# Optimization experiments

Measured on AMD Instinct MI355X. Metric: run time of the kernel, lower is better.

The kernel has to match this reference:

```python
import jax, jax.numpy as jnp
import numpy as np

B, C_IN, C_OUT, H, MAXN = 128, 32, 32, 4096, 6


def setup_inputs() -> dict:
    key = jax.random.key(0)
    ks = jax.random.split(key, 6)
    x = jax.random.normal(ks[0], (B, C_IN, H), dtype=jnp.float32)
    weight = jax.random.normal(ks[1], (C_OUT, C_IN, MAXN + 1), dtype=jnp.float32) * 0.05
    bias = jax.random.normal(ks[2], (C_OUT,), dtype=jnp.float32) * 0.05
    gamma = jnp.ones((C_OUT,), dtype=jnp.float32)
    beta = jnp.zeros((C_OUT,), dtype=jnp.float32)
    # hex neighbor table; -1 marks invalid (boundary) neighbors
    neighbors = jax.random.randint(ks[3], (H, MAXN), -1, H, dtype=jnp.int64)
    return {"x": x, "weight": weight, "bias": bias, "gamma": gamma,
            "beta": beta, "neighbors": neighbors, "groups": 1}


def reference(x, weight, bias, gamma, beta, neighbors, groups):
    Bsz, Cin, Hn = x.shape
    Cout, _, K = weight.shape  # K = total_inputs = max_neighbors + 1
    G = groups
    # global std normalization (torch std: unbiased, ddof=1)
    x = x / (jnp.std(x, ddof=1) + 1e-5)
    valid = (neighbors >= 0)                      # [H, K-1]
    idx = jnp.clip(neighbors, 0, None)
    nbr = x[:, :, idx] * valid.astype(x.dtype)[None, None]   # [B,C,H,K-1]
    allv = jnp.concatenate([x[..., None], nbr], axis=3)      # [B,C,H,K]
    allv = allv.reshape(Bsz, G, Cin // G, Hn, K)
    w = weight.reshape(G, Cout // G, Cin // G, K)
    out = jnp.einsum('bgihk,goik->bgoh', allv, w).reshape(Bsz, Cout, Hn)
    total_valid = valid.sum(axis=1).astype(out.dtype)[None, None] + 1.0  # [1,1,H]
    out = out / (total_valid + 1e-6)
    out = out + bias[None, :, None]
    # BatchNorm1d in training mode: per-channel over (batch, hex), biased var
    mean = out.mean(axis=(0, 2), keepdims=True)
    var = out.var(axis=(0, 2), keepdims=True)
    out = gamma[None, :, None] * (out - mean) * jax.lax.rsqrt(var + 1e-5) + beta[None, :, None]
    return out
```

## Files before the change

kernel.cpp:

```cpp
#include <hip/hip_runtime.h>
#include <stdint.h>
#include <stddef.h>

#define BSZ 128
#define CIN 32
#define COUT 32
#define HN 4096
#define K7 7
#define NTOT (BSZ*CIN*HN)
#define NBH  (BSZ*HN)

typedef __attribute__((ext_vector_type(8))) short short8;
typedef __attribute__((ext_vector_type(4))) float f32x4;

#define WS_XT   0
#define WS_WT   33554432
#define WS_NBR  33568768
#define WS_INVD 33699840
#define WS_DSP  33716224
#define WS_OST  33720320
#define WS_OSTP 33720576

__device__ __forceinline__ unsigned short f32_to_bf16(float f){
    union { float f; uint32_t u; } v; v.f = f;
    uint32_t u = v.u;
    return (unsigned short)((u + 0x7FFFu + ((u >> 16) & 1u)) >> 16);
}

__global__ void kprep(const int* __restrict__ nbr,
                      int* __restrict__ nbr_pack,
                      float* __restrict__ invd,
                      double* __restrict__ dsp,
                      float* __restrict__ ostatp){
    int t = blockIdx.x*blockDim.x + threadIdx.x;
    if (t < 512) dsp[t] = 0.0;
    #pragma unroll
    for (int j = 0; j < 4; j++) ostatp[t*4 + j] = 0.0f;
    if (t < HN){
        int cnt = 0;
        int pk[8];
        pk[0] = t;
        #pragma unroll
        for (int j = 0; j < 6; j++){
            int iv = nbr[t*6 + j];
            if (iv >= HN) iv = HN - 1;
            if (iv >= 0) cnt++; else iv = -1;
            pk[1+j] = iv;
        }
        pk[7] = 0;
        #pragma unroll
        for (int j = 0; j < 8; j++) nbr_pack[t*8 + j] = pk[j];
        invd[t] = 1.0f / ((float)cnt + 1.0f + 1e-6f);
    }
}

__global__ void ktrans(const float* __restrict__ x,
                       unsigned short* __restrict__ xt,
                       double* __restrict__ dsp){
    __shared__ float tile[32][65];
    __shared__ double red[8];
    int b  = blockIdx.x >> 6;
    int h0 = (blockIdx.x & 63) << 6;
    int t  = threadIdx.x;
    int hh = t & 63;
    int cq = t >> 6;
    double ds = 0.0, ds2 = 0.0;
    #pragma unroll
    for (int rep = 0; rep < 8; rep++){
        int c = rep*4 + cq;
        float v = x[((size_t)(b*32 + c))*HN + h0 + hh];
        tile[c][hh] = v;
        double dv = (double)v;
        ds += dv; ds2 += dv*dv;
    }
    #pragma unroll
    for (int off = 32; off; off >>= 1){
        ds  += __shfl_down(ds,  off);
        ds2 += __shfl_down(ds2, off);
    }
    int lane = t & 63, wv = t >> 6;
    if (lane == 0){ red[wv] = ds; red[4+wv] = ds2; }
    __syncthreads();
    if (t == 0){
        int slot = blockIdx.x & 255;
        atomicAdd(&dsp[slot*2],     red[0]+red[1]+red[2]+red[3]);
        atomicAdd(&dsp[slot*2 + 1], red[4]+red[5]+red[6]+red[7]);
    }
    int hw = t >> 2;
    int cg = (t & 3) * 8;
    alignas(16) unsigned short tmp[8];
    #pragma unroll
    for (int j = 0; j < 8; j++) tmp[j] = f32_to_bf16(tile[cg + j][hw]);
    *(uint4*)(xt + ((size_t)(b*HN + h0 + hw))*32 + cg) = *(const uint4*)tmp;
}

__global__ void kwt(const float* __restrict__ w,
                    const double* __restrict__ dsp,
                    unsigned short* __restrict__ wt){
    __shared__ double sred[8];
    __shared__ float sinv;
    int t = threadIdx.x;
    double d0 = dsp[t*2], d1 = dsp[t*2 + 1];
    #pragma unroll
    for (int off = 32; off; off >>= 1){
        d0 += __shfl_down(d0, off);
        d1 += __shfl_down(d1, off);
    }
    int lane = t & 63, wv = t >> 6;
    if (lane == 0){ sred[wv] = d0; sred[4+wv] = d1; }
    __syncthreads();
    if (t == 0){
        double sum   = sred[0]+sred[1]+sred[2]+sred[3];
        double sumsq = sred[4]+sred[5]+sred[6]+sred[7];
        double mean = sum / (double)NTOT;
        double var  = (sumsq - (double)NTOT*mean*mean) / (double)(NTOT - 1);
        sinv = 1.0f / ((float)sqrt(var) + 1e-5f);
    }
    __syncthreads();
    float inv_s = sinv;
    for (int i = t; i < COUT*K7*CIN; i += blockDim.x){
        int o  = i / (K7*CIN);
        int kk = (i / CIN) % K7;
        int c  = i % CIN;
        float val = w[(o*CIN + c)*K7 + kk] * inv_s;
        wt[i] = f32_to_bf16(val);
    }
}

__global__ __launch_bounds__(256) void kconv(
    const unsigned short* __restrict__ xt,
    const unsigned short* __restrict__ wt,
    const int* __restrict__ nbrp,
    const float* __restrict__ invd,
    const float* __restrict__ bias,
    float* __restrict__ out,
    float* __restrict__ ostatp)
{
    int lane = threadIdx.x & 63;
    int wv   = threadIdx.x >> 6;
    int wgid = blockIdx.x*4 + wv;
    int n    = lane & 15;
    int quad = lane >> 4;

    short8 af[2][K7];
    #pragma unroll
    for (int mt = 0; mt < 2; mt++){
        int o = n + 16*mt;
        #pragma unroll
        for (int kk = 0; kk < K7; kk++)
            af[mt][kk] = *(const short8*)(wt + (size_t)(o*K7 + kk)*CIN + quad*8);
    }
    float bias8[2][4];
    #pragma unroll
    for (int mt = 0; mt < 2; mt++)
        #pragma unroll
        for (int r = 0; r < 4; r++)
            bias8[mt][r] = bias[mt*16 + quad*4 + r];

    float sacc[8]  = {0,0,0,0,0,0,0,0};
    float sacc2[8] = {0,0,0,0,0,0,0,0};
    const short8 zero8 = {0,0,0,0,0,0,0,0};

    for (int tilei = wgid; tilei < (NBH/16); tilei += 8192){
        int b  = tilei >> 8;
        int h0 = (tilei & 255) << 4;
        int h  = h0 + n;
        float idv = invd[h];
        const int* np = nbrp + h*8;

        short8 bfr[K7];
        #pragma unroll
        for (int kk = 0; kk < K7; kk++){
            int row  = np[kk];
            int rowc = row < 0 ? 0 : row;
            bfr[kk] = *(const short8*)(xt + ((size_t)(b*HN + rowc))*32 + quad*8);
            if (row < 0) bfr[kk] = zero8;
        }
        f32x4 acc0 = {0.f,0.f,0.f,0.f};
        f32x4 acc1 = {0.f,0.f,0.f,0.f};
        #pragma unroll
        for (int kk = 0; kk < K7; kk++){
            acc0 = __builtin_amdgcn_mfma_f32_16x16x32_bf16(af[0][kk], bfr[kk], acc0, 0, 0, 0);
            acc1 = __builtin_amdgcn_mfma_f32_16x16x32_bf16(af[1][kk], bfr[kk], acc1, 0, 0, 0);
        }
        #pragma unroll
        for (int mt = 0; mt < 2; mt++){
            f32x4 a = mt ? acc1 : acc0;
            #pragma unroll
            for (int r = 0; r < 4; r++){
                int o = mt*16 + quad*4 + r;
                float v = a[r]*idv + bias8[mt][r];
                out[((size_t)(b*COUT + o))*HN + h] = v;
                sacc[mt*4 + r]  += v;
                sacc2[mt*4 + r] += v*v;
            }
        }
    }
    #pragma unroll
    for (int bit = 1; bit < 16; bit <<= 1){
        #pragma unroll
        for (int i = 0; i < 8; i++){
            sacc[i]  += __shfl_xor(sacc[i],  bit);
            sacc2[i] += __shfl_xor(sacc2[i], bit);
        }
    }
    if (n == 0){
        int slot = blockIdx.x & 255;
        #pragma unroll
        for (int mt = 0; mt < 2; mt++)
            #pragma unroll
            for (int r = 0; r < 4; r++){
                int o = mt*16 + quad*4 + r;
                atomicAdd(&ostatp[slot*64 + o],      sacc[mt*4 + r]);
                atomicAdd(&ostatp[slot*64 + 32 + o], sacc2[mt*4 + r]);
            }
    }
}

__global__ void kred(const float* __restrict__ ostatp,
                     float* __restrict__ ostat){
    __shared__ float part[4][64];
    int t = threadIdx.x;
    int a = t & 63;
    int g = t >> 6;
    float s = 0.0f;
    #pragma unroll
    for (int j = 0; j < 64; j++)
        s += ostatp[(g*64 + j)*64 + a];
    part[g][a] = s;
    __syncthreads();
    if (t < 64)
        ostat[t] = part[0][t] + part[1][t] + part[2][t] + part[3][t];
}

__global__ void kbn(float4* __restrict__ out4,
                    const float* __restrict__ ostat,
                    const float* __restrict__ gamma,
                    const float* __restrict__ beta){
    __shared__ float sc[32], sh[32];
    int t = threadIdx.x;
    if (t < 32){
        float mean = ostat[t] * (1.0f/(float)NBH);
        float var  = ostat[32 + t] * (1.0f/(float)NBH) - mean*mean;
        float s = gamma[t] * rsqrtf(var + 1e-5f);
        sc[t] = s;
        sh[t] = beta[t] - mean*s;
    }
    __syncthreads();
    int gid    = blockIdx.x*blockDim.x + t;
    int stride = gridDim.x*blockDim.x;
    for (int i = gid; i < NTOT/4; i += stride){
        int o = (i >> 10) & 31;
        float4 v = out4[i];
        float s = sc[o], b = sh[o];
        v.x = v.x*s + b; v.y = v.y*s + b; v.z = v.z*s + b; v.w = v.w*s + b;
        out4[i] = v;
    }
}

extern "C" void kernel_launch(void* const* d_in, const int* in_sizes, int n_in,
                              void* d_out, int out_size, void* d_ws, size_t ws_size,
                              hipStream_t stream) {
    const float* x      = (const float*)d_in[0];
    const float* weight = (const float*)d_in[1];
    const float* bias   = (const float*)d_in[2];
    const float* gamma  = (const float*)d_in[3];
    const float* beta   = (const float*)d_in[4];
    const int*   nbr    = (const int*)d_in[5];

    char* ws = (char*)d_ws;
    unsigned short* xt    = (unsigned short*)(ws + WS_XT);
    unsigned short* wt    = (unsigned short*)(ws + WS_WT);
    int*            nbrp  = (int*)(ws + WS_NBR);
    float*          invd  = (float*)(ws + WS_INVD);
    double*         dsp   = (double*)(ws + WS_DSP);
    float*          ostat = (float*)(ws + WS_OST);
    float*          ostatp= (float*)(ws + WS_OSTP);
    float*          out   = (float*)d_out;

    kprep <<<16,   256, 0, stream>>>(nbr, nbrp, invd, dsp, ostatp);
    ktrans<<<8192, 256, 0, stream>>>(x, xt, dsp);
    kwt   <<<1,    256, 0, stream>>>(weight, dsp, wt);
    kconv <<<2048, 256, 0, stream>>>(xt, wt, nbrp, invd, bias, out, ostatp);
    kred  <<<1,    256, 0, stream>>>(ostatp, ostat);
    kbn   <<<2048, 256, 0, stream>>>((float4*)out, ostat, gamma, beta);
}
```

Baseline: 204.1 us.

## Drop global std scaling and bias using BN invariance, store conv output as bf16

```diff
diff --git a/kernel.cpp b/kernel.cpp
--- a/kernel.cpp
+++ b/kernel.cpp
@@ -13,117 +13,81 @@
 typedef __attribute__((ext_vector_type(8))) short short8;
 typedef __attribute__((ext_vector_type(4))) float f32x4;
 
-#define WS_XT   0
+#define WS_OB   0
 #define WS_WT   33554432
 #define WS_NBR  33568768
 #define WS_INVD 33699840
-#define WS_DSP  33716224
-#define WS_OST  33720320
-#define WS_OSTP 33720576
+#define WS_OSTP 33716224
+#define WS_OST  33781760
 
 __device__ __forceinline__ unsigned short f32_to_bf16(float f){
     union { float f; uint32_t u; } v; v.f = f;
     uint32_t u = v.u;
     return (unsigned short)((u + 0x7FFFu + ((u >> 16) & 1u)) >> 16);
 }
-
-__global__ void kprep(const int* __restrict__ nbr,
+__device__ __forceinline__ float bf16_to_f32(unsigned short h){
+    union { uint32_t u; float f; } v; v.u = ((uint32_t)h) << 16;
+    return v.f;
+}
+
+__global__ void kinit(const int* __restrict__ nbr,
+                      const float* __restrict__ w,
                       int* __restrict__ nbr_pack,
                       float* __restrict__ invd,
-                      double* __restrict__ dsp,
+                      unsigned short* __restrict__ wt,
                       float* __restrict__ ostatp){
-    int t = blockIdx.x*blockDim.x + threadIdx.x;
-    if (t < 512) dsp[t] = 0.0;
-    #pragma unroll
-    for (int j = 0; j < 4; j++) ostatp[t*4 + j] = 0.0f;
-    if (t < HN){
+    int t = threadIdx.x;
+    if (blockIdx.x < 16){
+        int h = blockIdx.x*256 + t;
+        #pragma unroll
+        for (int j = 0; j < 4; j++) ostatp[h*4 + j] = 0.0f;
         int cnt = 0;
         int pk[8];
-        pk[0] = t;
         #pragma unroll
         for (int j = 0; j < 6; j++){
-            int iv = nbr[t*6 + j];
+            int iv = nbr[h*6 + j];
             if (iv >= HN) iv = HN - 1;
             if (iv >= 0) cnt++; else iv = -1;
-            pk[1+j] = iv;
-        }
-        pk[7] = 0;
-        #pragma unroll
-        for (int j = 0; j < 8; j++) nbr_pack[t*8 + j] = pk[j];
-        invd[t] = 1.0f / ((float)cnt + 1.0f + 1e-6f);
+            pk[j] = iv;
+        }
+        pk[6] = cnt; pk[7] = 0;
+        #pragma unroll
+        for (int j = 0; j < 8; j++) nbr_pack[h*8 + j] = pk[j];
+        invd[h] = 1.0f / ((float)cnt + 1.0f + 1e-6f);
+    } else {
+        for (int i = t; i < COUT*K7*CIN; i += 256){
+            int o  = i / (K7*CIN);
+            int kk = (i / CIN) % K7;
+            int c  = i % CIN;
+            wt[i] = f32_to_bf16(w[(o*CIN + c)*K7 + kk]);
+        }
     }
 }
 
 __global__ void ktrans(const float* __restrict__ x,
-                       unsigned short* __restrict__ xt,
-                       double* __restrict__ dsp){
-    __shared__ float tile[32][65];
-    __shared__ double red[8];
-    int b  = blockIdx.x >> 6;
-    int h0 = (blockIdx.x & 63) << 6;
+                       unsigned short* __restrict__ xt){
+    __shared__ float tile[32][260];
+    int b  = blockIdx.x >> 4;
+    int h0 = (blockIdx.x & 15) << 8;
     int t  = threadIdx.x;
-    int hh = t & 63;
-    int cq = t >> 6;
-    double ds = 0.0, ds2 = 0.0;
-    #pragma unroll
-    for (int rep = 0; rep < 8; rep++){
-        int c = rep*4 + cq;
-        float v = x[((size_t)(b*32 + c))*HN + h0 + hh];
-        tile[c][hh] = v;
-        double dv = (double)v;
-        ds += dv; ds2 += dv*dv;
-    }
-    #pragma unroll
-    for (int off = 32; off; off >>= 1){
-        ds  += __shfl_down(ds,  off);
-        ds2 += __shfl_down(ds2, off);
-    }
-    int lane = t & 63, wv = t >> 6;
-    if (lane == 0){ red[wv] = ds; red[4+wv] = ds2; }
+    #pragma unroll
+    for (int l = 0; l < 8; l++){
+        int linear = l*256 + t;
+        int c  = linear >> 6;
+        int h4 = linear & 63;
+        float4 v = *(const float4*)(x + ((size_t)(b*CIN + c))*HN + h0 + h4*4);
+        *(float4*)&tile[c][h4*4] = v;
+    }
     __syncthreads();
-    if (t == 0){
-        int slot = blockIdx.x & 255;
-        atomicAdd(&dsp[slot*2],     red[0]+red[1]+red[2]+red[3]);
-        atomicAdd(&dsp[slot*2 + 1], red[4]+red[5]+red[6]+red[7]);
-    }
+    int cg = (t & 3) * 8;
     int hw = t >> 2;
-    int cg = (t & 3) * 8;
-    alignas(16) unsigned short tmp[8];
-    #pragma unroll
-    for (int j = 0; j < 8; j++) tmp[j] = f32_to_bf16(tile[cg + j][hw]);
-    *(uint4*)(xt + ((size_t)(b*HN + h0 + hw))*32 + cg) = *(const uint4*)tmp;
-}
-
-__global__ void kwt(const float* __restrict__ w,
-                    const double* __restrict__ dsp,
-                    unsigned short* __restrict__ wt){
-    __shared__ double sred[8];
-    __shared__ float sinv;
-    int t = threadIdx.x;
-    double d0 = dsp[t*2], d1 = dsp[t*2 + 1];
-    #pragma unroll
-    for (int off = 32; off; off >>= 1){
-        d0 += __shfl_down(d0, off);
-        d1 += __shfl_down(d1, off);
-    }
-    int lane = t & 63, wv = t >> 6;
-    if (lane == 0){ sred[wv] = d0; sred[4+wv] = d1; }
-    __syncthreads();
-    if (t == 0){
-        double sum   = sred[0]+sred[1]+sred[2]+sred[3];
-        double sumsq = sred[4]+sred[5]+sred[6]+sred[7];
-        double mean = sum / (double)NTOT;
-        double var  = (sumsq - (double)NTOT*mean*mean) / (double)(NTOT - 1);
-        sinv = 1.0f / ((float)sqrt(var) + 1e-5f);
-    }
-    __syncthreads();
-    float inv_s = sinv;
-    for (int i = t; i < COUT*K7*CIN; i += blockDim.x){
-        int o  = i / (K7*CIN);
-        int kk = (i / CIN) % K7;
-        int c  = i % CIN;
-        float val = w[(o*CIN + c)*K7 + kk] * inv_s;
-        wt[i] = f32_to_bf16(val);
+    #pragma unroll
+    for (int r = 0; r < 4; r++){
+        int h = r*64 + hw;
+        alignas(16) unsigned short tmp[8];
+        #pragma unroll
+        for (int j = 0; j < 8; j++) tmp[j] = f32_to_bf16(tile[cg + j][h]);
+        *(uint4*)(xt + ((size_t)(b*HN + h0 + h))*32 + cg) = *(const uint4*)tmp;
     }
 }
 
@@ -132,15 +96,17 @@
     const unsigned short* __restrict__ wt,
     const int* __restrict__ nbrp,
     const float* __restrict__ invd,
-    const float* __restrict__ bias,
-    float* __restrict__ out,
+    unsigned short* __restrict__ ob,
     float* __restrict__ ostatp)
 {
     int lane = threadIdx.x & 63;
     int wv   = threadIdx.x >> 6;
-    int wgid = blockIdx.x*4 + wv;
     int n    = lane & 15;
     int quad = lane >> 4;
+    int xcd  = blockIdx.x & 7;
+    int j    = blockIdx.x >> 3;
+    int b    = xcd*16 + (j >> 4);
+    int hbase= ((j & 15)*4 + wv) * 64;
 
     short8 af[2][K7];
     #pragma unroll
@@ -150,31 +116,34 @@
         for (int kk = 0; kk < K7; kk++)
             af[mt][kk] = *(const short8*)(wt + (size_t)(o*K7 + kk)*CIN + quad*8);
     }
-    float bias8[2][4];
-    #pragma unroll
-    for (int mt = 0; mt < 2; mt++)
-        #pragma unroll
-        for (int r = 0; r < 4; r++)
-            bias8[mt][r] = bias[mt*16 + quad*4 + r];
 
     float sacc[8]  = {0,0,0,0,0,0,0,0};
     float sacc2[8] = {0,0,0,0,0,0,0,0};
     const short8 zero8 = {0,0,0,0,0,0,0,0};
-
-    for (int tilei = wgid; tilei < (NBH/16); tilei += 8192){
-        int b  = tilei >> 8;
-        int h0 = (tilei & 255) << 4;
-        int h  = h0 + n;
-        float idv = invd[h];
-        const int* np = nbrp + h*8;
+    const unsigned short* xb = xt + (size_t)b*HN*CIN;
+
+    int h = hbase + n;
+    int4 na = *(const int4*)(nbrp + h*8);
+    int4 nb = *(const int4*)(nbrp + h*8 + 4);
+    float idv = invd[h];
+
+    #pragma unroll 1
+    for (int it = 0; it < 4; it++){
+        int hc = hbase + it*16 + n;
+        int hn = hbase + (it < 3 ? it+1 : it)*16 + n;
+        int4 na2 = *(const int4*)(nbrp + hn*8);
+        int4 nb2 = *(const int4*)(nbrp + hn*8 + 4);
+        float idv2 = invd[hn];
 
         short8 bfr[K7];
-        #pragma unroll
-        for (int kk = 0; kk < K7; kk++){
-            int row  = np[kk];
+        bfr[0] = *(const short8*)(xb + (size_t)hc*CIN + quad*8);
+        int rows[6] = {na.x, na.y, na.z, na.w, nb.x, nb.y};
+        #pragma unroll
+        for (int kk = 0; kk < 6; kk++){
+            int row  = rows[kk];
             int rowc = row < 0 ? 0 : row;
-            bfr[kk] = *(const short8*)(xt + ((size_t)(b*HN + rowc))*32 + quad*8);
-            if (row < 0) bfr[kk] = zero8;
+            bfr[kk+1] = *(const short8*)(xb + (size_t)rowc*CIN + quad*8);
+            if (row < 0) bfr[kk+1] = zero8;
         }
         f32x4 acc0 = {0.f,0.f,0.f,0.f};
         f32x4 acc1 = {0.f,0.f,0.f,0.f};
@@ -189,12 +158,13 @@
             #pragma unroll
             for (int r = 0; r < 4; r++){
                 int o = mt*16 + quad*4 + r;
-                float v = a[r]*idv + bias8[mt][r];
-                out[((size_t)(b*COUT + o))*HN + h] = v;
+                float v = a[r]*idv;
+                ob[((size_t)(b*COUT + o))*HN + hc] = f32_to_bf16(v);
                 sacc[mt*4 + r]  += v;
                 sacc2[mt*4 + r] += v*v;
             }
         }
+        na = na2; nb = nb2; idv = idv2;
     }
     #pragma unroll
     for (int bit = 1; bit < 16; bit <<= 1){
@@ -233,7 +203,8 @@
         ostat[t] = part[0][t] + part[1][t] + part[2][t] + part[3][t];
 }
 
-__global__ void kbn(float4* __restrict__ out4,
+__global__ void kbn(const unsigned short* __restrict__ ob,
+                    float* __restrict__ out,
                     const float* __restrict__ ostat,
                     const float* __restrict__ gamma,
                     const float* __restrict__ beta){
@@ -249,12 +220,22 @@
     __syncthreads();
     int gid    = blockIdx.x*blockDim.x + t;
     int stride = gridDim.x*blockDim.x;
-    for (int i = gid; i < NTOT/4; i += stride){
-        int o = (i >> 10) & 31;
-        float4 v = out4[i];
-        float s = sc[o], b = sh[o];
-        v.x = v.x*s + b; v.y = v.y*s + b; v.z = v.z*s + b; v.w = v.w*s + b;
-        out4[i] = v;
+    for (int i = gid; i < NTOT/8; i += stride){
+        int o = (i >> 9) & 31;
+        uint4 raw = ((const uint4*)ob)[i];
+        const unsigned short* p = (const unsigned short*)&raw;
+        float s = sc[o], bsh = sh[o];
+        float4 r0, r1;
+        r0.x = bf16_to_f32(p[0])*s + bsh;
+        r0.y = bf16_to_f32(p[1])*s + bsh;
+        r0.z = bf16_to_f32(p[2])*s + bsh;
+        r0.w = bf16_to_f32(p[3])*s + bsh;
+        r1.x = bf16_to_f32(p[4])*s + bsh;
+        r1.y = bf16_to_f32(p[5])*s + bsh;
+        r1.z = bf16_to_f32(p[6])*s + bsh;
+        r1.w = bf16_to_f32(p[7])*s + bsh;
+        ((float4*)out)[i*2]     = r0;
+        ((float4*)out)[i*2 + 1] = r1;
     }
 }
 
@@ -263,25 +244,23 @@
                               hipStream_t stream) {
     const float* x      = (const float*)d_in[0];
     const float* weight = (const float*)d_in[1];
-    const float* bias   = (const float*)d_in[2];
     const float* gamma  = (const float*)d_in[3];
     const float* beta   = (const float*)d_in[4];
     const int*   nbr    = (const int*)d_in[5];
 
     char* ws = (char*)d_ws;
-    unsigned short* xt    = (unsigned short*)(ws + WS_XT);
+    unsigned short* ob    = (unsigned short*)(ws + WS_OB);
     unsigned short* wt    = (unsigned short*)(ws + WS_WT);
     int*            nbrp  = (int*)(ws + WS_NBR);
     float*          invd  = (float*)(ws + WS_INVD);
-    double*         dsp   = (double*)(ws + WS_DSP);
+    float*          ostatp= (float*)(ws + WS_OSTP);
     float*          ostat = (float*)(ws + WS_OST);
-    float*          ostatp= (float*)(ws + WS_OSTP);
     float*          out   = (float*)d_out;
-
-    kprep <<<16,   256, 0, stream>>>(nbr, nbrp, invd, dsp, ostatp);
-    ktrans<<<8192, 256, 0, stream>>>(x, xt, dsp);
-    kwt   <<<1,    256, 0, stream>>>(weight, dsp, wt);
-    kconv <<<2048, 256, 0, stream>>>(xt, wt, nbrp, invd, bias, out, ostatp);
+    unsigned short* xt    = (unsigned short*)d_out + 16777216;
+
+    kinit <<<17,   256, 0, stream>>>(nbr, weight, nbrp, invd, wt, ostatp);
+    ktrans<<<2048, 256, 0, stream>>>(x, xt);
+    kconv <<<2048, 256, 0, stream>>>(xt, wt, nbrp, invd, ob, ostatp);
     kred  <<<1,    256, 0, stream>>>(ostatp, ostat);
-    kbn   <<<2048, 256, 0, stream>>>((float4*)out, ostat, gamma, beta);
-}
+    kbn   <<<2048, 256, 0, stream>>>(ob, out, ostat, gamma, beta);
+}
```

Result: faster. 184.9 us (-9.4%).
